# Optimization experiments

Measured on AMD Instinct MI355X. Metric: run time of the kernel, lower is better.

## Reference

```python
import jax, jax.numpy as jnp
import numpy as np


def setup_inputs() -> dict:
    key = jax.random.key(0)
    k1, k2 = jax.random.split(key)
    N, D = 8192, 200
    preds = jax.random.normal(k1, (N, 1, 1, D), dtype=jnp.float32)
    labels = jax.random.randint(k2, (N,), 0, 64, dtype=jnp.int64)
    return {"preds": preds, "labels": labels}


def reference(preds, labels):
    # preds: (N,1,1,200) -> flatten to (N,200); torch.dist is the L2 norm of the
    # elementwise difference over the whole tensor.
    N = preds.shape[0]
    x = preds.reshape(N, -1).astype(jnp.float32)
    sq = jnp.sum(x * x, axis=-1)                      # (N,)
    gram = x @ x.T                                    # (N,N)
    d2 = sq[:, None] + sq[None, :] - 2.0 * gram       # squared pairwise dist
    eye = jnp.eye(N, dtype=bool)
    # keep diagonal out of the sqrt (it is skipped by the i==j continue)
    d2_safe = jnp.where(eye, 1.0, jnp.maximum(d2, 0.0))
    dist = jnp.sqrt(d2_safe)                          # (N,N)
    sign = jnp.where(labels[:, None] == labels[None, :], 1.0, -1.0)
    sign = jnp.where(eye, 0.0, sign)
    # each pred_loss[i] is a (1,1,200) tensor filled with the scalar s_i,
    # so the final mean over the stack equals mean_i(s_i).
    per_i = jnp.sum(sign * dist, axis=1)              # (N,)
    return jnp.mean(per_i)
```

## Files before the change

### kernel.cpp

```cpp
#include <hip/hip_runtime.h>
#include <hip/hip_fp8.h>

#define N 8192
#define D 200
#define KP 232
#define NSTEP 7
#define TB 128
#define NT 64
#define TPP 65
#define NBLK (32 * TPP)
#define PANEL (TB * KP)
#define NCELL 256

typedef float f32x4 __attribute__((ext_vector_type(4)));
#define AS3 __attribute__((address_space(3)))
#define AS1 __attribute__((address_space(1)))

__global__ __launch_bounds__(256) void prep_kernel(
    const float* __restrict__ x, const int* __restrict__ labels,
    unsigned char* __restrict__ xb, float* __restrict__ sq,
    int* __restrict__ lab, double* __restrict__ cells) {
  if (blockIdx.x == 0) cells[threadIdx.x] = 0.0;
  int row = blockIdx.x * 4 + (threadIdx.x >> 6);
  int lane = threadIdx.x & 63;
  const float* xr = x + (size_t)row * D;
  unsigned char* xbr = xb + (size_t)row * KP;
  int k0 = lane * 4;
  float4 f = {0.f, 0.f, 0.f, 0.f};
  if (k0 < D) f = *(const float4*)(xr + k0);
  float s = 0.f;
  unsigned char q[4];
  float ff[4] = {f.x, f.y, f.z, f.w};
#pragma unroll
  for (int c = 0; c < 4; ++c) {
    float v = (k0 + c < D) ? ff[c] : 0.f;
    __hip_fp8_e4m3 h(v);
    q[c] = h.__x;
    float fb = (float)h;
    s += fb * fb;
  }
  if (k0 < KP) *(uchar4*)(xbr + k0) = *(uchar4*)q;
#pragma unroll
  for (int m = 32; m; m >>= 1) s += __shfl_xor(s, m);
  if (lane == 0) {
    sq[row] = s;
    lab[row] = labels[row];
  }
}

__global__ __launch_bounds__(512, 4) void gram_kernel(
    const unsigned char* __restrict__ xb, const float* __restrict__ sq,
    const int* __restrict__ lab, double* __restrict__ cells) {
  __shared__ __align__(16) unsigned char sA[PANEL];
  __shared__ __align__(16) unsigned char sB[PANEL];

  const int t = threadIdx.x;
  const int b = (blockIdx.x & 7) * (NBLK / 8) + (blockIdx.x >> 3);
  const int q = b / TPP, idx = b - q * TPP;
  const int n1 = NT - q;
  const int I = (idx < n1) ? q : NT - 1 - q;
  const int J = (idx < n1) ? q + idx : (NT - 1 - q) + (idx - n1);

  auto stage = [&](const unsigned char* g, unsigned char* sh) {
#pragma unroll
    for (int c = 0; c < 3; ++c) {
      int off = c * 8192 + t * 16;
      __builtin_amdgcn_global_load_lds((const AS1 void*)(g + off),
                                       (AS3 void*)(sh + off), 16, 0, 0);
    }
    if (t < 320) {
      int off = 24576 + t * 16;
      __builtin_amdgcn_global_load_lds((const AS1 void*)(g + off),
                                       (AS3 void*)(sh + off), 16, 0, 0);
    }
  };
  stage(xb + (size_t)I * PANEL, sA);
  stage(xb + (size_t)J * PANEL, sB);

  const int wid = t >> 6, lane = t & 63;
  const int col = lane & 15, quad = lane >> 4;
  const int waveM = (wid & 1) * 64, waveN = (wid >> 1) * 32;
  const int i0 = I * TB + waveM, j0 = J * TB + waveN;
  int labj[2];
  float sqj[2];
#pragma unroll
  for (int ni = 0; ni < 2; ++ni) {
    int j = j0 + ni * 16 + col;
    labj[ni] = lab[j];
    sqj[ni] = sq[j];
  }
  float4 sqi4[4];
  int4 li4[4];
#pragma unroll
  for (int mi = 0; mi < 4; ++mi) {
    sqi4[mi] = *(const float4*)(sq + i0 + mi * 16 + quad * 4);
    li4[mi] = *(const int4*)(lab + i0 + mi * 16 + quad * 4);
  }
  __syncthreads();

  f32x4 acc[4][2] = {};
  __builtin_amdgcn_s_setprio(1);
#pragma unroll
  for (int step = 0; step < NSTEP; ++step) {
    long a[4], bf[2];
#pragma unroll
    for (int mi = 0; mi < 4; ++mi)
      a[mi] = *(const long*)(sA + (waveM + mi * 16 + col) * KP + step * 32 + quad * 8);
#pragma unroll
    for (int ni = 0; ni < 2; ++ni)
      bf[ni] = *(const long*)(sB + (waveN + ni * 16 + col) * KP + step * 32 + quad * 8);
#pragma unroll
    for (int mi = 0; mi < 4; ++mi)
#pragma unroll
      for (int ni = 0; ni < 2; ++ni)
        acc[mi][ni] = __builtin_amdgcn_mfma_f32_16x16x32_fp8_fp8(
            a[mi], bf[ni], acc[mi][ni], 0, 0, 0);
  }
  __builtin_amdgcn_s_setprio(0);

  float rs = 0.f, tot;
  if (I != J) {
#pragma unroll
    for (int mi = 0; mi < 4; ++mi) {
      float sqi[4] = {sqi4[mi].x, sqi4[mi].y, sqi4[mi].z, sqi4[mi].w};
      int li[4] = {li4[mi].x, li4[mi].y, li4[mi].z, li4[mi].w};
#pragma unroll
      for (int r = 0; r < 4; ++r)
#pragma unroll
        for (int ni = 0; ni < 2; ++ni) {
          float g = acc[mi][ni][r];
          float d2 = fmaxf(fmaf(-2.f, g, sqi[r] + sqj[ni]), 0.f);
          float dist = __builtin_amdgcn_sqrtf(d2);
          rs += (li[r] == labj[ni]) ? dist : -dist;
        }
    }
    tot = 2.f * rs;
  } else {
#pragma unroll
    for (int mi = 0; mi < 4; ++mi) {
      float sqi[4] = {sqi4[mi].x, sqi4[mi].y, sqi4[mi].z, sqi4[mi].w};
      int li[4] = {li4[mi].x, li4[mi].y, li4[mi].z, li4[mi].w};
#pragma unroll
      for (int r = 0; r < 4; ++r) {
        int i = i0 + mi * 16 + quad * 4 + r;
#pragma unroll
        for (int ni = 0; ni < 2; ++ni) {
          int j = j0 + ni * 16 + col;
          float g = acc[mi][ni][r];
          float d2 = fmaxf(fmaf(-2.f, g, sqi[r] + sqj[ni]), 0.f);
          float dist = __builtin_amdgcn_sqrtf(d2);
          float c = (li[r] == labj[ni]) ? dist : -dist;
          rs += (i == j) ? 0.f : c;
        }
      }
    }
    tot = rs;
  }

#pragma unroll
  for (int m = 32; m; m >>= 1) tot += __shfl_xor(tot, m);
  if (lane == 0)
    atomicAdd(&cells[(b * 8 + wid) & (NCELL - 1)], (double)tot);
}

__global__ __launch_bounds__(256) void reduce_kernel(
    const double* __restrict__ cells, float* __restrict__ out) {
  __shared__ double wsum[4];
  double s = cells[threadIdx.x];
#pragma unroll
  for (int m = 32; m; m >>= 1) s += __shfl_xor(s, m);
  if ((threadIdx.x & 63) == 0) wsum[threadIdx.x >> 6] = s;
  __syncthreads();
  if (threadIdx.x == 0)
    out[0] = (float)((wsum[0] + wsum[1] + wsum[2] + wsum[3]) / (double)N);
}

extern "C" void kernel_launch(void* const* d_in, const int* in_sizes, int n_in,
                              void* d_out, int out_size, void* d_ws, size_t ws_size,
                              hipStream_t stream) {
  const float* x = (const float*)d_in[0];
  const int* labels = (const int*)d_in[1];
  char* ws = (char*)d_ws;
  unsigned char* xb = (unsigned char*)ws;
  float* sq = (float*)(ws + (size_t)N * KP);
  int* lab = (int*)(ws + (size_t)N * KP + (size_t)N * 4);
  double* cells = (double*)(ws + (size_t)N * KP + (size_t)N * 8);
  float* out = (float*)d_out;

  prep_kernel<<<N / 4, 256, 0, stream>>>(x, labels, xb, sq, lab, cells);
  gram_kernel<<<NBLK, 512, 0, stream>>>(xb, sq, lab, cells);
  reduce_kernel<<<1, 256, 0, stream>>>(cells, out);
}
```

Before: 85.00 us.

## Use 128x64 gram tiles with 256-thread blocks and unified upper-triangle masking

Replaces the 128x128 tiles (512 threads, 2080 blocks) with 128x64 tiles handled by 256 threads, giving 4160 blocks and a smaller LDS footprint per block. The triangular tile enumeration is remapped so each block covers a 128-row panel against a 64-column panel, with the diagonal and off-diagonal epilogues merged into one path that masks to gi<gj and doubles the sum. This is meant to improve occupancy and load balance, at the cost of more redundant A-panel loads and a per-element compare in every tile.

```diff
diff --git a/kernel.cpp b/kernel.cpp
--- a/kernel.cpp
+++ b/kernel.cpp
@@ -5,11 +5,9 @@
 #define D 200
 #define KP 232
 #define NSTEP 7
-#define TB 128
-#define NT 64
-#define TPP 65
-#define NBLK (32 * TPP)
-#define PANEL (TB * KP)
+#define NBLK 4160
+#define PANEL_A (128 * KP)
+#define PANEL_B (64 * KP)
 #define NCELL 256
 
 typedef float f32x4 __attribute__((ext_vector_type(4)));
@@ -48,39 +46,52 @@
   }
 }
 
-__global__ __launch_bounds__(512, 4) void gram_kernel(
+__global__ __launch_bounds__(256, 3) void gram_kernel(
     const unsigned char* __restrict__ xb, const float* __restrict__ sq,
     const int* __restrict__ lab, double* __restrict__ cells) {
-  __shared__ __align__(16) unsigned char sA[PANEL];
-  __shared__ __align__(16) unsigned char sB[PANEL];
+  __shared__ __align__(16) unsigned char sA[PANEL_A];
+  __shared__ __align__(16) unsigned char sB[PANEL_B];
 
   const int t = threadIdx.x;
   const int b = (blockIdx.x & 7) * (NBLK / 8) + (blockIdx.x >> 3);
-  const int q = b / TPP, idx = b - q * TPP;
-  const int n1 = NT - q;
-  const int I = (idx < n1) ? q : NT - 1 - q;
-  const int J = (idx < n1) ? q + idx : (NT - 1 - q) + (idx - n1);
+  const int pr = b / 130, r = b - pr * 130;
+  const int n1 = 128 - 2 * pr;
+  const int q  = (r < n1) ? pr : 63 - pr;
+  const int j2 = (r < n1) ? 2 * pr + r : 2 * (63 - pr) + (r - n1);
 
-  auto stage = [&](const unsigned char* g, unsigned char* sh) {
+  auto stageA = [&](const unsigned char* g) {
+#pragma unroll
+    for (int c = 0; c < 7; ++c) {
+      int off = c * 4096 + t * 16;
+      __builtin_amdgcn_global_load_lds((const AS1 void*)(g + off),
+                                       (AS3 void*)(sA + off), 16, 0, 0);
+    }
+    if (t < 64) {
+      int off = 28672 + t * 16;
+      __builtin_amdgcn_global_load_lds((const AS1 void*)(g + off),
+                                       (AS3 void*)(sA + off), 16, 0, 0);
+    }
+  };
+  auto stageB = [&](const unsigned char* g) {
 #pragma unroll
     for (int c = 0; c < 3; ++c) {
-      int off = c * 8192 + t * 16;
+      int off = c * 4096 + t * 16;
       __builtin_amdgcn_global_load_lds((const AS1 void*)(g + off),
-                                       (AS3 void*)(sh + off), 16, 0, 0);
+                                       (AS3 void*)(sB + off), 16, 0, 0);
     }
-    if (t < 320) {
-      int off = 24576 + t * 16;
+    if (t < 160) {
+      int off = 12288 + t * 16;
       __builtin_amdgcn_global_load_lds((const AS1 void*)(g + off),
-                                       (AS3 void*)(sh + off), 16, 0, 0);
+                                       (AS3 void*)(sB + off), 16, 0, 0);
     }
   };
-  stage(xb + (size_t)I * PANEL, sA);
-  stage(xb + (size_t)J * PANEL, sB);
+  stageA(xb + (size_t)q * PANEL_A);
+  stageB(xb + (size_t)j2 * PANEL_B);
 
   const int wid = t >> 6, lane = t & 63;
   const int col = lane & 15, quad = lane >> 4;
   const int waveM = (wid & 1) * 64, waveN = (wid >> 1) * 32;
-  const int i0 = I * TB + waveM, j0 = J * TB + waveN;
+  const int i0 = q * 128 + waveM, j0 = j2 * 64 + waveN;
   int labj[2];
   float sqj[2];
 #pragma unroll
@@ -118,49 +129,31 @@
   }
   __builtin_amdgcn_s_setprio(0);
 
-  float rs = 0.f, tot;
-  if (I != J) {
+  float rs = 0.f;
 #pragma unroll
-    for (int mi = 0; mi < 4; ++mi) {
-      float sqi[4] = {sqi4[mi].x, sqi4[mi].y, sqi4[mi].z, sqi4[mi].w};
-      int li[4] = {li4[mi].x, li4[mi].y, li4[mi].z, li4[mi].w};
+  for (int mi = 0; mi < 4; ++mi) {
+    float sqi[4] = {sqi4[mi].x, sqi4[mi].y, sqi4[mi].z, sqi4[mi].w};
+    int li[4] = {li4[mi].x, li4[mi].y, li4[mi].z, li4[mi].w};
 #pragma unroll
-      for (int r = 0; r < 4; ++r)
+    for (int r4 = 0; r4 < 4; ++r4) {
+      int gi = i0 + mi * 16 + quad * 4 + r4;
 #pragma unroll
-        for (int ni = 0; ni < 2; ++ni) {
-          float g = acc[mi][ni][r];
-          float d2 = fmaxf(fmaf(-2.f, g, sqi[r] + sqj[ni]), 0.f);
-          float dist = __builtin_amdgcn_sqrtf(d2);
-          rs += (li[r] == labj[ni]) ? dist : -dist;
-        }
-    }
-    tot = 2.f * rs;
-  } else {
-#pragma unroll
-    for (int mi = 0; mi < 4; ++mi) {
-      float sqi[4] = {sqi4[mi].x, sqi4[mi].y, sqi4[mi].z, sqi4[mi].w};
-      int li[4] = {li4[mi].x, li4[mi].y, li4[mi].z, li4[mi].w};
-#pragma unroll
-      for (int r = 0; r < 4; ++r) {
-        int i = i0 + mi * 16 + quad * 4 + r;
-#pragma unroll
-        for (int ni = 0; ni < 2; ++ni) {
-          int j = j0 + ni * 16 + col;
-          float g = acc[mi][ni][r];
-          float d2 = fmaxf(fmaf(-2.f, g, sqi[r] + sqj[ni]), 0.f);
-          float dist = __builtin_amdgcn_sqrtf(d2);
-          float c = (li[r] == labj[ni]) ? dist : -dist;
-          rs += (i == j) ? 0.f : c;
-        }
+      for (int ni = 0; ni < 2; ++ni) {
+        int gj = j0 + ni * 16 + col;
+        float g = acc[mi][ni][r4];
+        float d2 = fmaxf(fmaf(-2.f, g, sqi[r4] + sqj[ni]), 0.f);
+        float dist = __builtin_amdgcn_sqrtf(d2);
+        float c = (li[r4] == labj[ni]) ? dist : -dist;
+        rs += (gi < gj) ? c : 0.f;
       }
     }
-    tot = rs;
   }
+  float tot = 2.f * rs;
 
 #pragma unroll
   for (int m = 32; m; m >>= 1) tot += __shfl_xor(tot, m);
   if (lane == 0)
-    atomicAdd(&cells[(b * 8 + wid) & (NCELL - 1)], (double)tot);
+    atomicAdd(&cells[(b * 4 + wid) & (NCELL - 1)], (double)tot);
 }
 
 __global__ __launch_bounds__(256) void reduce_kernel(
@@ -188,6 +181,6 @@
   float* out = (float*)d_out;
 
   prep_kernel<<<N / 4, 256, 0, stream>>>(x, labels, xb, sq, lab, cells);
-  gram_kernel<<<NBLK, 512, 0, stream>>>(xb, sq, lab, cells);
+  gram_kernel<<<NBLK, 256, 0, stream>>>(xb, sq, lab, cells);
   reduce_kernel<<<1, 256, 0, stream>>>(cells, out);
 }
```

New measurement: 83.87 us. No clear change (-1.3%).
